# Optimization experiments

Measured on AMD Instinct MI355X. Metric: run time of the kernel, lower is better.

## Reference

```python
import math
import jax, jax.numpy as jnp
import numpy as np

jax.config.update("jax_enable_x64", True)

# ---- module hyperparameters (init_kwargs) ----
BS, NDIM, NSTEP, ORDER = 16, 16, 128, 2
NIV, NIVSTEPS = 2, 1
P = ORDER + 1                 # number of derivative channels u^(0)..u^(order)
N = NSTEP * P                 # unknowns per system
FACT = np.array([math.factorial(k) for k in range(P)], dtype=np.float64)

# Hard initial-value constraint matrix C (same sparsity for every system)
_C = np.zeros((NIVSTEPS * NIV, N), dtype=np.float64)
for _t in range(NIVSTEPS):
    for _i in range(NIV):
        _C[_t * NIV + _i, _t * P + _i] = 1.0
C = jnp.asarray(_C)
NC = C.shape[0]


def setup_inputs() -> dict:
    key = jax.random.key(0)
    k1, k2, k3, k4 = jax.random.split(key, 4)
    coeffs = jax.random.normal(k1, (BS, NDIM, NSTEP, P), dtype=jnp.float32)
    rhs = jax.random.normal(k2, (BS, NDIM, NSTEP), dtype=jnp.float32)
    iv_rhs = jax.random.normal(k3, (BS, NDIM, NIVSTEPS, NIV), dtype=jnp.float32)
    # step sizes must be positive; keep them in [0.1, 0.2] for good conditioning
    steps = 0.1 + 0.1 * jax.random.uniform(k4, (BS, NDIM, NSTEP - 1), dtype=jnp.float32)
    return {"coeffs": coeffs, "rhs": rhs, "iv_rhs": iv_rhs, "steps": steps}


def _build_A(coeffs, h):
    """Soft-constraint matrix for one scalar ODE system.
    coeffs: (NSTEP, P) f64   ODE coefficients per step
    h:      (NSTEP-1,) f64   step sizes
    Rows: [equation | fwd/bwd Taylor smoothness per order | top-order diff].
    Smoothness rows are normalized by the local truncation error h^(order+1-i).
    """
    n = NSTEP
    t = jnp.arange(n - 1)
    # equation constraints: sum_i c[t,i] u[t,i] = rhs[t]
    A_eq = jnp.zeros((n, N)).at[jnp.repeat(jnp.arange(n), P), jnp.arange(N)].set(coeffs.ravel())
    blocks = [A_eq]
    for i in range(ORDER):
        scale = h ** (-(ORDER + 1 - i))          # (n-1,)
        Af = jnp.zeros((n - 1, N))
        Ab = jnp.zeros((n - 1, N))
        for j in range(i, P):
            cf = (h ** (j - i)) / FACT[j - i]
            cb = ((-h) ** (j - i)) / FACT[j - i]
            Af = Af.at[t, t * P + j].set(scale * cf)        # forward Taylor from step t
            Ab = Ab.at[t, (t + 1) * P + j].set(scale * cb)  # backward Taylor from step t+1
        Af = Af.at[t, (t + 1) * P + i].set(-scale)
        Ab = Ab.at[t, t * P + i].set(-scale)
        blocks += [Af, Ab]
    # highest derivative varies slowly: (u[t+1,K] - u[t,K]) / h ~ 0
    Atop = (jnp.zeros((n - 1, N))
            .at[t, (t + 1) * P + ORDER].set(1.0 / h)
            .at[t, t * P + ORDER].set(-1.0 / h))
    blocks.append(Atop)
    return jnp.concatenate(blocks, axis=0)   # (m, N), m = n + 2(n-1)K + (n-1)


def _solve_one(coeffs, rhs, iv, h):
    """min ||A u - b||^2  s.t.  C u = iv  (KKT solve), one system."""
    A = _build_A(coeffs, h)
    m = A.shape[0]
    b = jnp.concatenate([rhs, jnp.zeros(m - NSTEP)])
    G = A.T @ A                                  # (N, N) banded normal matrix
    Atb = A.T @ b
    M = jnp.block([[G, C.T], [C, jnp.zeros((NC, NC))]])
    v = jnp.concatenate([Atb, iv.ravel()])
    x = jnp.linalg.solve(M, v)
    return x[:N].reshape(NSTEP, P)


def reference(coeffs, rhs, iv_rhs, steps):
    coeffs64 = coeffs.reshape(BS, NDIM, NSTEP, P).astype(jnp.float64)
    rhs64 = rhs.reshape(BS, NDIM, NSTEP).astype(jnp.float64)
    iv64 = iv_rhs.reshape(BS, NDIM, NIVSTEPS, NIV).astype(jnp.float64)
    h64 = steps.reshape(BS, NDIM, NSTEP - 1).astype(jnp.float64)
    solve = jax.vmap(jax.vmap(_solve_one))
    u = solve(coeffs64, rhs64, iv64, h64)        # (BS, NDIM, NSTEP, P)
    u0, u1, u2 = u[..., 0], u[..., 1], u[..., 2]
    return (u0, u1, u2, jnp.zeros(()), h64.reshape(BS * NDIM, NSTEP - 1, 1))
```

## Files before the change

### kernel.cpp

```cpp
#include <hip/hip_runtime.h>

#define NSYS_ 256

__device__ __forceinline__ void sym_inv3(const double D[9], double Dinv[9]) {
    const double a = D[0], b = D[3], c = D[4], d = D[6], e = D[7], f = D[8];
    const double A00 = c*f - e*e;
    const double A01 = d*e - b*f;
    const double A02 = b*e - c*d;
    const double A11 = a*f - d*d;
    const double A12 = b*d - a*e;
    const double A22 = a*c - b*b;
    const double det  = a*A00 + b*A01 + d*A02;
    const double idet = 1.0 / det;
    Dinv[0] = A00*idet; Dinv[1] = A01*idet; Dinv[2] = A02*idet;
    Dinv[3] = A01*idet; Dinv[4] = A11*idet; Dinv[5] = A12*idet;
    Dinv[6] = A02*idet; Dinv[7] = A12*idet; Dinv[8] = A22*idet;
}

__device__ __forceinline__ void iface_rows(double h, double wL[5][3], double wR[5][3]) {
    const double ih = 1.0 / h;
    const double s1 = ih * ih;
    const double s0 = s1 * ih;
    const double hh = 0.5 * ih;
    wL[0][0]= s0; wL[0][1]= s1; wL[0][2]= hh;  wR[0][0]=-s0; wR[0][1]=0.0; wR[0][2]=0.0;
    wL[1][0]=-s0; wL[1][1]=0.0; wL[1][2]=0.0;  wR[1][0]= s0; wR[1][1]=-s1; wR[1][2]= hh;
    wL[2][0]=0.0; wL[2][1]= s1; wL[2][2]= ih;  wR[2][0]=0.0; wR[2][1]=-s1; wR[2][2]=0.0;
    wL[3][0]=0.0; wL[3][1]=-s1; wL[3][2]=0.0;  wR[3][0]=0.0; wR[3][1]= s1; wR[3][2]=-ih;
    wL[4][0]=0.0; wL[4][1]=0.0; wL[4][2]=-ih;  wR[4][0]=0.0; wR[4][1]=0.0; wR[4][2]= ih;
}

__global__ __launch_bounds__(64)
void ode_pcr_1wave(const float* __restrict__ coeffs,
                   const float* __restrict__ rhs,
                   const float* __restrict__ ivr,
                   const float* __restrict__ steps,
                   float* __restrict__ out)
{
    const int sys = blockIdx.x;
    const int l   = threadIdx.x;
    const int m0  = 2*l, m1 = 2*l+1;

    const float* cP  = coeffs + (size_t)sys * 384;
    const float* rP  = rhs    + (size_t)sys * 128;
    const float* ivP = ivr    + (size_t)sys * 2;
    const float* hP  = steps  + (size_t)sys * 127;

    __shared__ double ex[2][18][64];

    const float hf0 = hP[m0];
    const float hf1 = (l < 63) ? hP[m1] : 0.0f;

    double D0[9], U0[9], r0[3], D1[9], U1[9], r1[3];
    {
        const double c0[3] = {(double)cP[m0*3+0], (double)cP[m0*3+1], (double)cP[m0*3+2]};
        const double c1[3] = {(double)cP[m1*3+0], (double)cP[m1*3+1], (double)cP[m1*3+2]};
        const double rv0 = (double)rP[m0], rv1 = (double)rP[m1];
        #pragma unroll
        for (int a=0;a<3;++a){
          #pragma unroll
          for (int b=0;b<3;++b){ D0[a*3+b]=c0[a]*c0[b]; D1[a*3+b]=c1[a]*c1[b];
                                 U0[a*3+b]=0.0;        U1[a*3+b]=0.0; }
          r0[a]=c0[a]*rv0; r1[a]=c1[a]*rv1;
        }
    }
    {
        double wL[5][3], wR[5][3];
        iface_rows((double)hf0, wL, wR);
        #pragma unroll
        for (int k=0;k<5;++k)
          #pragma unroll
          for (int a=0;a<3;++a)
            #pragma unroll
            for (int b=0;b<3;++b){
              D0[a*3+b] += wL[k][a]*wL[k][b];
              U0[a*3+b] += wL[k][a]*wR[k][b];
              D1[a*3+b] += wR[k][a]*wR[k][b];
            }
    }
    if (l >= 1) {
        double wL[5][3], wR[5][3];
        iface_rows((double)hP[m0-1], wL, wR);
        #pragma unroll
        for (int k=0;k<5;++k)
          #pragma unroll
          for (int a=0;a<3;++a)
            #pragma unroll
            for (int b=0;b<3;++b)
              D0[a*3+b] += wR[k][a]*wR[k][b];
    }
    if (l < 63) {
        double wL[5][3], wR[5][3];
        iface_rows((double)hf1, wL, wR);
        #pragma unroll
        for (int k=0;k<5;++k)
          #pragma unroll
          for (int a=0;a<3;++a)
            #pragma unroll
            for (int b=0;b<3;++b){
              D1[a*3+b] += wL[k][a]*wL[k][b];
              U1[a*3+b] += wL[k][a]*wR[k][b];
            }
    }
    if (l == 0) {
        const double iv0 = (double)ivP[0], iv1 = (double)ivP[1];
        #pragma unroll
        for (int b=0;b<3;++b) r1[b] -= U0[0*3+b]*iv0 + U0[1*3+b]*iv1;
        #pragma unroll
        for (int b=0;b<3;++b){ U0[0*3+b]=0.0; U0[1*3+b]=0.0; }
        r0[2] -= D0[6]*iv0 + D0[7]*iv1;
        r0[0] = iv0; r0[1] = iv1;
        D0[1]=D0[2]=D0[3]=D0[5]=D0[6]=D0[7]=0.0;
        D0[0]=1.0; D0[4]=1.0;
    }

    double TA[9], TB[9], z1[3];
    {
        double Dinv1[9]; sym_inv3(D1, Dinv1);
        #pragma unroll
        for (int a=0;a<3;++a)
          #pragma unroll
          for (int k=0;k<3;++k){
            double s=0.0, s2=0.0;
            #pragma unroll
            for (int j=0;j<3;++j){ s  += U0[a*3+j]*Dinv1[j*3+k];
                                   s2 += Dinv1[a*3+j]*U1[j*3+k]; }
            TA[a*3+k]=s; TB[a*3+k]=s2;
          }
        #pragma unroll
        for (int j=0;j<3;++j)
          z1[j] = Dinv1[j*3+0]*r1[0] + Dinv1[j*3+1]*r1[1] + Dinv1[j*3+2]*r1[2];
    }
    double D[9], U[9], r[3];
    #pragma unroll
    for (int a=0;a<3;++a){
      #pragma unroll
      for (int b=0;b<3;++b){
        double sd=0.0, su=0.0;
        #pragma unroll
        for (int j=0;j<3;++j){ sd += TA[a*3+j]*U0[b*3+j];
                               su += TA[a*3+j]*U1[j*3+b]; }
        D[a*3+b] = D0[a*3+b] - sd;
        U[a*3+b] = -su;
      }
      r[a] = r0[a] - (TA[a*3+0]*r1[0] + TA[a*3+1]*r1[1] + TA[a*3+2]*r1[2]);
    }
    {
        double Cn[9], cn[3];
        #pragma unroll
        for (int a=0;a<3;++a){
          #pragma unroll
          for (int b=0;b<3;++b){
            double s=0.0;
            #pragma unroll
            for (int j=0;j<3;++j) s += U1[j*3+a]*TB[j*3+b];
            Cn[a*3+b]=s;
          }
          cn[a] = U1[0*3+a]*z1[0] + U1[1*3+a]*z1[1] + U1[2*3+a]*z1[2];
        }
        ex[0][0][l]=Cn[0]; ex[0][1][l]=Cn[1]; ex[0][2][l]=Cn[2];
        ex[0][3][l]=Cn[4]; ex[0][4][l]=Cn[5]; ex[0][5][l]=Cn[8];
        ex[0][6][l]=cn[0]; ex[0][7][l]=cn[1]; ex[0][8][l]=cn[2];
    }
    __syncthreads();
    if (l >= 1) {
        const int p = l-1;
        const double C0=ex[0][0][p], C1=ex[0][1][p], C2=ex[0][2][p],
                     C3=ex[0][3][p], C4=ex[0][4][p], C5=ex[0][5][p];
        D[0]-=C0; D[1]-=C1; D[2]-=C2;
        D[3]-=C1; D[4]-=C3; D[5]-=C4;
        D[6]-=C2; D[7]-=C4; D[8]-=C5;
        r[0]-=ex[0][6][p]; r[1]-=ex[0][7][p]; r[2]-=ex[0][8][p];
    }
    __syncthreads();

    int s = 0;
    for (int d = 1; d < 64; d <<= 1, ++s) {
        double Dinv[9]; sym_inv3(D, Dinv);
        double (*buf)[64] = ex[s & 1];
        buf[0][l]=Dinv[0]; buf[1][l]=Dinv[1]; buf[2][l]=Dinv[2];
        buf[3][l]=Dinv[4]; buf[4][l]=Dinv[5]; buf[5][l]=Dinv[8];
        #pragma unroll
        for (int i=0;i<9;++i) buf[6+i][l]=U[i];
        buf[15][l]=r[0]; buf[16][l]=r[1]; buf[17][l]=r[2];
        __syncthreads();

        double nD[9], nU[9], nr[3];
        #pragma unroll
        for (int i=0;i<9;++i){ nD[i]=D[i]; nU[i]=0.0; }
        nr[0]=r[0]; nr[1]=r[1]; nr[2]=r[2];

        if (l + d < 64) {
            const int p = l + d;
            double Dp[9], Up[9], rp[3];
            Dp[0]=buf[0][p]; Dp[1]=buf[1][p]; Dp[2]=buf[2][p];
            Dp[3]=Dp[1];     Dp[4]=buf[3][p]; Dp[5]=buf[4][p];
            Dp[6]=Dp[2];     Dp[7]=Dp[5];     Dp[8]=buf[5][p];
            #pragma unroll
            for (int i=0;i<9;++i) Up[i]=buf[6+i][p];
            rp[0]=buf[15][p]; rp[1]=buf[16][p]; rp[2]=buf[17][p];
            double Tp[9];
            #pragma unroll
            for (int a=0;a<3;++a)
              #pragma unroll
              for (int k=0;k<3;++k)
                Tp[a*3+k] = U[a*3+0]*Dp[0*3+k] + U[a*3+1]*Dp[1*3+k] + U[a*3+2]*Dp[2*3+k];
            #pragma unroll
            for (int a=0;a<3;++a){
              #pragma unroll
              for (int b=0;b<3;++b){
                double su=0.0, sd=0.0;
                #pragma unroll
                for (int j=0;j<3;++j){ su += Tp[a*3+j]*Up[j*3+b]; sd += Tp[a*3+j]*U[b*3+j]; }
                nU[a*3+b] = -su;
                nD[a*3+b] -= sd;
              }
              nr[a] -= Tp[a*3+0]*rp[0] + Tp[a*3+1]*rp[1] + Tp[a*3+2]*rp[2];
            }
        }
        if (l - d >= 0) {
            const int p = l - d;
            double Dm[9], Um[9], rm[3];
            Dm[0]=buf[0][p]; Dm[1]=buf[1][p]; Dm[2]=buf[2][p];
            Dm[3]=Dm[1];     Dm[4]=buf[3][p]; Dm[5]=buf[4][p];
            Dm[6]=Dm[2];     Dm[7]=Dm[5];     Dm[8]=buf[5][p];
            #pragma unroll
            for (int i=0;i<9;++i) Um[i]=buf[6+i][p];
            rm[0]=buf[15][p]; rm[1]=buf[16][p]; rm[2]=buf[17][p];
            double Tm[9];
            #pragma unroll
            for (int a=0;a<3;++a)
              #pragma unroll
              for (int k=0;k<3;++k)
                Tm[a*3+k] = Um[0*3+a]*Dm[0*3+k] + Um[1*3+a]*Dm[1*3+k] + Um[2*3+a]*Dm[2*3+k];
            #pragma unroll
            for (int a=0;a<3;++a){
              #pragma unroll
              for (int b=0;b<3;++b){
                double sd=0.0;
                #pragma unroll
                for (int j=0;j<3;++j) sd += Tm[a*3+j]*Um[j*3+b];
                nD[a*3+b] -= sd;
              }
              nr[a] -= Tm[a*3+0]*rm[0] + Tm[a*3+1]*rm[1] + Tm[a*3+2]*rm[2];
            }
        }
        #pragma unroll
        for (int i=0;i<9;++i){ D[i]=nD[i]; U[i]=nU[i]; }
        r[0]=nr[0]; r[1]=nr[1]; r[2]=nr[2];
    }

    double Dinv[9]; sym_inv3(D, Dinv);
    const double xe0 = Dinv[0]*r[0] + Dinv[1]*r[1] + Dinv[2]*r[2];
    const double xe1 = Dinv[3]*r[0] + Dinv[4]*r[1] + Dinv[5]*r[2];
    const double xe2 = Dinv[6]*r[0] + Dinv[7]*r[1] + Dinv[8]*r[2];
    ex[0][0][l]=xe0; ex[0][1][l]=xe1; ex[0][2][l]=xe2;
    __syncthreads();
    double xN[3] = {0.0, 0.0, 0.0};
    if (l < 63) { xN[0]=ex[0][0][l+1]; xN[1]=ex[0][1][l+1]; xN[2]=ex[0][2][l+1]; }
    double xo[3];
    #pragma unroll
    for (int j=0;j<3;++j)
        xo[j] = z1[j] - (TA[0*3+j]*xe0 + TA[1*3+j]*xe1 + TA[2*3+j]*xe2)
                      - (TB[j*3+0]*xN[0] + TB[j*3+1]*xN[1] + TB[j*3+2]*xN[2]);

    float2* o0 = (float2*)(out)         + (size_t)sys*64;
    float2* o1 = (float2*)(out + 32768) + (size_t)sys*64;
    float2* o2 = (float2*)(out + 65536) + (size_t)sys*64;
    o0[l] = make_float2((float)xe0, (float)xo[0]);
    o1[l] = make_float2((float)xe1, (float)xo[1]);
    o2[l] = make_float2((float)xe2, (float)xo[2]);
    float* outH = out + 98305 + (size_t)sys*127;
    outH[m0] = hf0;
    if (l < 63) outH[m1] = hf1;
    if (sys == 0 && l == 0) out[98304] = 0.0f;
}

extern "C" void kernel_launch(void* const* d_in, const int* in_sizes, int n_in,
                              void* d_out, int out_size, void* d_ws, size_t ws_size,
                              hipStream_t stream) {
    const float* coeffs = (const float*)d_in[0];
    const float* rhs    = (const float*)d_in[1];
    const float* ivr    = (const float*)d_in[2];
    const float* steps  = (const float*)d_in[3];
    float* out = (float*)d_out;
    (void)in_sizes; (void)n_in; (void)out_size; (void)d_ws; (void)ws_size;
    hipLaunchKernelGGL(ode_pcr_1wave, dim3(NSYS_), dim3(64), 0, stream,
                       coeffs, rhs, ivr, steps, out);
}
```

Before: 12.05 us.

## Exploit symmetry, fast reciprocal, wave shuffles, and skip last-step U update in PCR

Replaces the double-precision divisions with a hardware reciprocal refined by two Newton steps, and computes only the lower triangle of the symmetric diagonal blocks. The initial interface reduction and the final back-substitution now exchange values with wave shuffles instead of shared memory and barriers. The last PCR level skips the off-diagonal update it does not need, and the step-size output is written early. These cut FP64 arithmetic and synchronisation cost; the risks are slightly different rounding and reliance on a 64-lane wave.

After: 12.12 us. About the same (+0.6%).

```diff
diff --git a/kernel.cpp b/kernel.cpp
--- a/kernel.cpp
+++ b/kernel.cpp
@@ -1,6 +1,16 @@
 #include <hip/hip_runtime.h>
+#include <math.h>
 
 #define NSYS_ 256
+
+__device__ __forceinline__ double frcp(double x) {
+    double r = __builtin_amdgcn_rcp(x);
+    double e = fma(-x, r, 1.0);
+    r = fma(r, e, r);
+    e = fma(-x, r, 1.0);
+    r = fma(r, e, r);
+    return r;
+}
 
 __device__ __forceinline__ void sym_inv3(const double D[9], double Dinv[9]) {
     const double a = D[0], b = D[3], c = D[4], d = D[6], e = D[7], f = D[8];
@@ -11,14 +21,14 @@
     const double A12 = b*d - a*e;
     const double A22 = a*c - b*b;
     const double det  = a*A00 + b*A01 + d*A02;
-    const double idet = 1.0 / det;
+    const double idet = frcp(det);
     Dinv[0] = A00*idet; Dinv[1] = A01*idet; Dinv[2] = A02*idet;
-    Dinv[3] = A01*idet; Dinv[4] = A11*idet; Dinv[5] = A12*idet;
-    Dinv[6] = A02*idet; Dinv[7] = A12*idet; Dinv[8] = A22*idet;
+    Dinv[3] = Dinv[1];  Dinv[4] = A11*idet; Dinv[5] = A12*idet;
+    Dinv[6] = Dinv[2];  Dinv[7] = Dinv[5];  Dinv[8] = A22*idet;
 }
 
 __device__ __forceinline__ void iface_rows(double h, double wL[5][3], double wR[5][3]) {
-    const double ih = 1.0 / h;
+    const double ih = frcp(h);
     const double s1 = ih * ih;
     const double s0 = s1 * ih;
     const double hh = 0.5 * ih;
@@ -50,6 +60,13 @@
     const float hf0 = hP[m0];
     const float hf1 = (l < 63) ? hP[m1] : 0.0f;
 
+    {
+        float* outH = out + 98305 + (size_t)sys*127;
+        outH[m0] = hf0;
+        if (l < 63) outH[m1] = hf1;
+        if (sys == 0 && l == 0) out[98304] = 0.0f;
+    }
+
     double D0[9], U0[9], r0[3], D1[9], U1[9], r1[3];
     {
         const double c0[3] = {(double)cP[m0*3+0], (double)cP[m0*3+1], (double)cP[m0*3+2]};
@@ -58,8 +75,9 @@
         #pragma unroll
         for (int a=0;a<3;++a){
           #pragma unroll
-          for (int b=0;b<3;++b){ D0[a*3+b]=c0[a]*c0[b]; D1[a*3+b]=c1[a]*c1[b];
-                                 U0[a*3+b]=0.0;        U1[a*3+b]=0.0; }
+          for (int b=0;b<=a;++b){ D0[a*3+b]=c0[a]*c0[b]; D1[a*3+b]=c1[a]*c1[b]; }
+          #pragma unroll
+          for (int b=0;b<3;++b){ U0[a*3+b]=0.0; U1[a*3+b]=0.0; }
           r0[a]=c0[a]*rv0; r1[a]=c1[a]*rv1;
         }
     }
@@ -69,13 +87,16 @@
         #pragma unroll
         for (int k=0;k<5;++k)
           #pragma unroll
-          for (int a=0;a<3;++a)
-            #pragma unroll
-            for (int b=0;b<3;++b){
+          for (int a=0;a<3;++a){
+            #pragma unroll
+            for (int b=0;b<=a;++b){
               D0[a*3+b] += wL[k][a]*wL[k][b];
-              U0[a*3+b] += wL[k][a]*wR[k][b];
               D1[a*3+b] += wR[k][a]*wR[k][b];
             }
+            #pragma unroll
+            for (int b=0;b<3;++b)
+              U0[a*3+b] += wL[k][a]*wR[k][b];
+          }
     }
     if (l >= 1) {
         double wL[5][3], wR[5][3];
@@ -85,7 +106,7 @@
           #pragma unroll
           for (int a=0;a<3;++a)
             #pragma unroll
-            for (int b=0;b<3;++b)
+            for (int b=0;b<=a;++b)
               D0[a*3+b] += wR[k][a]*wR[k][b];
     }
     if (l < 63) {
@@ -94,12 +115,14 @@
         #pragma unroll
         for (int k=0;k<5;++k)
           #pragma unroll
-          for (int a=0;a<3;++a)
-            #pragma unroll
-            for (int b=0;b<3;++b){
+          for (int a=0;a<3;++a){
+            #pragma unroll
+            for (int b=0;b<=a;++b)
               D1[a*3+b] += wL[k][a]*wL[k][b];
+            #pragma unroll
+            for (int b=0;b<3;++b)
               U1[a*3+b] += wL[k][a]*wR[k][b];
-            }
+          }
     }
     if (l == 0) {
         const double iv0 = (double)ivP[0], iv1 = (double)ivP[1];
@@ -109,7 +132,7 @@
         for (int b=0;b<3;++b){ U0[0*3+b]=0.0; U0[1*3+b]=0.0; }
         r0[2] -= D0[6]*iv0 + D0[7]*iv1;
         r0[0] = iv0; r0[1] = iv1;
-        D0[1]=D0[2]=D0[3]=D0[5]=D0[6]=D0[7]=0.0;
+        D0[3]=0.0; D0[6]=0.0; D0[7]=0.0;
         D0[0]=1.0; D0[4]=1.0;
     }
 
@@ -120,11 +143,8 @@
         for (int a=0;a<3;++a)
           #pragma unroll
           for (int k=0;k<3;++k){
-            double s=0.0, s2=0.0;
-            #pragma unroll
-            for (int j=0;j<3;++j){ s  += U0[a*3+j]*Dinv1[j*3+k];
-                                   s2 += Dinv1[a*3+j]*U1[j*3+k]; }
-            TA[a*3+k]=s; TB[a*3+k]=s2;
+            TA[a*3+k] = U0[a*3+0]*Dinv1[0*3+k] + U0[a*3+1]*Dinv1[1*3+k] + U0[a*3+2]*Dinv1[2*3+k];
+            TB[a*3+k] = Dinv1[a*3+0]*U1[0*3+k] + Dinv1[a*3+1]*U1[1*3+k] + Dinv1[a*3+2]*U1[2*3+k];
           }
         #pragma unroll
         for (int j=0;j<3;++j)
@@ -134,47 +154,36 @@
     #pragma unroll
     for (int a=0;a<3;++a){
       #pragma unroll
-      for (int b=0;b<3;++b){
-        double sd=0.0, su=0.0;
-        #pragma unroll
-        for (int j=0;j<3;++j){ sd += TA[a*3+j]*U0[b*3+j];
-                               su += TA[a*3+j]*U1[j*3+b]; }
-        D[a*3+b] = D0[a*3+b] - sd;
-        U[a*3+b] = -su;
-      }
+      for (int b=0;b<=a;++b)
+        D[a*3+b] = D0[a*3+b] - (TA[a*3+0]*U0[b*3+0] + TA[a*3+1]*U0[b*3+1] + TA[a*3+2]*U0[b*3+2]);
+      #pragma unroll
+      for (int b=0;b<3;++b)
+        U[a*3+b] = -(TA[a*3+0]*U1[0*3+b] + TA[a*3+1]*U1[1*3+b] + TA[a*3+2]*U1[2*3+b]);
       r[a] = r0[a] - (TA[a*3+0]*r1[0] + TA[a*3+1]*r1[1] + TA[a*3+2]*r1[2]);
     }
     {
-        double Cn[9], cn[3];
-        #pragma unroll
-        for (int a=0;a<3;++a){
-          #pragma unroll
-          for (int b=0;b<3;++b){
-            double s=0.0;
-            #pragma unroll
-            for (int j=0;j<3;++j) s += U1[j*3+a]*TB[j*3+b];
-            Cn[a*3+b]=s;
-          }
-          cn[a] = U1[0*3+a]*z1[0] + U1[1*3+a]*z1[1] + U1[2*3+a]*z1[2];
-        }
-        ex[0][0][l]=Cn[0]; ex[0][1][l]=Cn[1]; ex[0][2][l]=Cn[2];
-        ex[0][3][l]=Cn[4]; ex[0][4][l]=Cn[5]; ex[0][5][l]=Cn[8];
-        ex[0][6][l]=cn[0]; ex[0][7][l]=cn[1]; ex[0][8][l]=cn[2];
-    }
-    __syncthreads();
-    if (l >= 1) {
-        const int p = l-1;
-        const double C0=ex[0][0][p], C1=ex[0][1][p], C2=ex[0][2][p],
-                     C3=ex[0][3][p], C4=ex[0][4][p], C5=ex[0][5][p];
-        D[0]-=C0; D[1]-=C1; D[2]-=C2;
-        D[3]-=C1; D[4]-=C3; D[5]-=C4;
-        D[6]-=C2; D[7]-=C4; D[8]-=C5;
-        r[0]-=ex[0][6][p]; r[1]-=ex[0][7][p]; r[2]-=ex[0][8][p];
-    }
-    __syncthreads();
-
-    int s = 0;
-    for (int d = 1; d < 64; d <<= 1, ++s) {
+        double q[9];
+        q[0] = U1[0]*TB[0] + U1[3]*TB[3] + U1[6]*TB[6];
+        q[1] = U1[1]*TB[0] + U1[4]*TB[3] + U1[7]*TB[6];
+        q[2] = U1[2]*TB[0] + U1[5]*TB[3] + U1[8]*TB[6];
+        q[3] = U1[1]*TB[1] + U1[4]*TB[4] + U1[7]*TB[7];
+        q[4] = U1[2]*TB[1] + U1[5]*TB[4] + U1[8]*TB[7];
+        q[5] = U1[2]*TB[2] + U1[5]*TB[5] + U1[8]*TB[8];
+        q[6] = U1[0]*z1[0] + U1[3]*z1[1] + U1[6]*z1[2];
+        q[7] = U1[1]*z1[0] + U1[4]*z1[1] + U1[7]*z1[2];
+        q[8] = U1[2]*z1[0] + U1[5]*z1[1] + U1[8]*z1[2];
+        double qi[9];
+        #pragma unroll
+        for (int i=0;i<9;++i) qi[i] = __shfl_up(q[i], 1);
+        if (l >= 1) {
+            D[0]-=qi[0]; D[3]-=qi[1]; D[6]-=qi[2]; D[4]-=qi[3]; D[7]-=qi[4]; D[8]-=qi[5];
+            r[0]-=qi[6]; r[1]-=qi[7]; r[2]-=qi[8];
+        }
+    }
+
+    #pragma unroll 1
+    for (int s = 0; s < 6; ++s) {
+        const int d = 1 << s;
         double Dinv[9]; sym_inv3(D, Dinv);
         double (*buf)[64] = ex[s & 1];
         buf[0][l]=Dinv[0]; buf[1][l]=Dinv[1]; buf[2][l]=Dinv[2];
@@ -184,68 +193,76 @@
         buf[15][l]=r[0]; buf[16][l]=r[1]; buf[17][l]=r[2];
         __syncthreads();
 
-        double nD[9], nU[9], nr[3];
-        #pragma unroll
-        for (int i=0;i<9;++i){ nD[i]=D[i]; nU[i]=0.0; }
-        nr[0]=r[0]; nr[1]=r[1]; nr[2]=r[2];
+        double nD[6] = { D[0], D[3], D[6], D[4], D[7], D[8] };
+        double nU[9];
+        #pragma unroll
+        for (int i=0;i<9;++i) nU[i]=0.0;
+        double nr[3] = { r[0], r[1], r[2] };
 
         if (l + d < 64) {
             const int p = l + d;
-            double Dp[9], Up[9], rp[3];
+            double Dp[9];
             Dp[0]=buf[0][p]; Dp[1]=buf[1][p]; Dp[2]=buf[2][p];
             Dp[3]=Dp[1];     Dp[4]=buf[3][p]; Dp[5]=buf[4][p];
             Dp[6]=Dp[2];     Dp[7]=Dp[5];     Dp[8]=buf[5][p];
-            #pragma unroll
-            for (int i=0;i<9;++i) Up[i]=buf[6+i][p];
-            rp[0]=buf[15][p]; rp[1]=buf[16][p]; rp[2]=buf[17][p];
-            double Tp[9];
+            const double rp0=buf[15][p], rp1=buf[16][p], rp2=buf[17][p];
+            double T[9];
             #pragma unroll
             for (int a=0;a<3;++a)
               #pragma unroll
               for (int k=0;k<3;++k)
-                Tp[a*3+k] = U[a*3+0]*Dp[0*3+k] + U[a*3+1]*Dp[1*3+k] + U[a*3+2]*Dp[2*3+k];
-            #pragma unroll
-            for (int a=0;a<3;++a){
-              #pragma unroll
-              for (int b=0;b<3;++b){
-                double su=0.0, sd=0.0;
+                T[a*3+k] = U[a*3+0]*Dp[0*3+k] + U[a*3+1]*Dp[1*3+k] + U[a*3+2]*Dp[2*3+k];
+            nD[0] -= T[0]*U[0] + T[1]*U[1] + T[2]*U[2];
+            nD[1] -= T[3]*U[0] + T[4]*U[1] + T[5]*U[2];
+            nD[2] -= T[6]*U[0] + T[7]*U[1] + T[8]*U[2];
+            nD[3] -= T[3]*U[3] + T[4]*U[4] + T[5]*U[5];
+            nD[4] -= T[6]*U[3] + T[7]*U[4] + T[8]*U[5];
+            nD[5] -= T[6]*U[6] + T[7]*U[7] + T[8]*U[8];
+            nr[0] -= T[0]*rp0 + T[1]*rp1 + T[2]*rp2;
+            nr[1] -= T[3]*rp0 + T[4]*rp1 + T[5]*rp2;
+            nr[2] -= T[6]*rp0 + T[7]*rp1 + T[8]*rp2;
+            if (s < 5) {
+                double Up[9];
                 #pragma unroll
-                for (int j=0;j<3;++j){ su += Tp[a*3+j]*Up[j*3+b]; sd += Tp[a*3+j]*U[b*3+j]; }
-                nU[a*3+b] = -su;
-                nD[a*3+b] -= sd;
-              }
-              nr[a] -= Tp[a*3+0]*rp[0] + Tp[a*3+1]*rp[1] + Tp[a*3+2]*rp[2];
+                for (int i=0;i<9;++i) Up[i]=buf[6+i][p];
+                #pragma unroll
+                for (int a=0;a<3;++a)
+                  #pragma unroll
+                  for (int b=0;b<3;++b)
+                    nU[a*3+b] = -(T[a*3+0]*Up[0*3+b] + T[a*3+1]*Up[1*3+b] + T[a*3+2]*Up[2*3+b]);
             }
         }
-        if (l - d >= 0) {
+        if (l >= d) {
             const int p = l - d;
-            double Dm[9], Um[9], rm[3];
+            double Dm[9];
             Dm[0]=buf[0][p]; Dm[1]=buf[1][p]; Dm[2]=buf[2][p];
             Dm[3]=Dm[1];     Dm[4]=buf[3][p]; Dm[5]=buf[4][p];
             Dm[6]=Dm[2];     Dm[7]=Dm[5];     Dm[8]=buf[5][p];
+            double Um[9];
             #pragma unroll
             for (int i=0;i<9;++i) Um[i]=buf[6+i][p];
-            rm[0]=buf[15][p]; rm[1]=buf[16][p]; rm[2]=buf[17][p];
+            const double rm0=buf[15][p], rm1=buf[16][p], rm2=buf[17][p];
             double Tm[9];
             #pragma unroll
             for (int a=0;a<3;++a)
               #pragma unroll
               for (int k=0;k<3;++k)
                 Tm[a*3+k] = Um[0*3+a]*Dm[0*3+k] + Um[1*3+a]*Dm[1*3+k] + Um[2*3+a]*Dm[2*3+k];
-            #pragma unroll
-            for (int a=0;a<3;++a){
-              #pragma unroll
-              for (int b=0;b<3;++b){
-                double sd=0.0;
-                #pragma unroll
-                for (int j=0;j<3;++j) sd += Tm[a*3+j]*Um[j*3+b];
-                nD[a*3+b] -= sd;
-              }
-              nr[a] -= Tm[a*3+0]*rm[0] + Tm[a*3+1]*rm[1] + Tm[a*3+2]*rm[2];
-            }
-        }
-        #pragma unroll
-        for (int i=0;i<9;++i){ D[i]=nD[i]; U[i]=nU[i]; }
+            nD[0] -= Tm[0]*Um[0] + Tm[1]*Um[3] + Tm[2]*Um[6];
+            nD[1] -= Tm[3]*Um[0] + Tm[4]*Um[3] + Tm[5]*Um[6];
+            nD[2] -= Tm[6]*Um[0] + Tm[7]*Um[3] + Tm[8]*Um[6];
+            nD[3] -= Tm[3]*Um[1] + Tm[4]*Um[4] + Tm[5]*Um[7];
+            nD[4] -= Tm[6]*Um[1] + Tm[7]*Um[4] + Tm[8]*Um[7];
+            nD[5] -= Tm[6]*Um[2] + Tm[7]*Um[5] + Tm[8]*Um[8];
+            nr[0] -= Tm[0]*rm0 + Tm[1]*rm1 + Tm[2]*rm2;
+            nr[1] -= Tm[3]*rm0 + Tm[4]*rm1 + Tm[5]*rm2;
+            nr[2] -= Tm[6]*rm0 + Tm[7]*rm1 + Tm[8]*rm2;
+        }
+        D[0]=nD[0]; D[3]=nD[1]; D[6]=nD[2]; D[4]=nD[3]; D[7]=nD[4]; D[8]=nD[5];
+        if (s < 5) {
+            #pragma unroll
+            for (int i=0;i<9;++i) U[i]=nU[i];
+        }
         r[0]=nr[0]; r[1]=nr[1]; r[2]=nr[2];
     }
 
@@ -253,15 +270,15 @@
     const double xe0 = Dinv[0]*r[0] + Dinv[1]*r[1] + Dinv[2]*r[2];
     const double xe1 = Dinv[3]*r[0] + Dinv[4]*r[1] + Dinv[5]*r[2];
     const double xe2 = Dinv[6]*r[0] + Dinv[7]*r[1] + Dinv[8]*r[2];
-    ex[0][0][l]=xe0; ex[0][1][l]=xe1; ex[0][2][l]=xe2;
-    __syncthreads();
-    double xN[3] = {0.0, 0.0, 0.0};
-    if (l < 63) { xN[0]=ex[0][0][l+1]; xN[1]=ex[0][1][l+1]; xN[2]=ex[0][2][l+1]; }
+    double xN0 = __shfl_down(xe0, 1);
+    double xN1 = __shfl_down(xe1, 1);
+    double xN2 = __shfl_down(xe2, 1);
+    if (l == 63) { xN0 = 0.0; xN1 = 0.0; xN2 = 0.0; }
     double xo[3];
     #pragma unroll
     for (int j=0;j<3;++j)
         xo[j] = z1[j] - (TA[0*3+j]*xe0 + TA[1*3+j]*xe1 + TA[2*3+j]*xe2)
-                      - (TB[j*3+0]*xN[0] + TB[j*3+1]*xN[1] + TB[j*3+2]*xN[2]);
+                      - (TB[j*3+0]*xN0 + TB[j*3+1]*xN1 + TB[j*3+2]*xN2);
 
     float2* o0 = (float2*)(out)         + (size_t)sys*64;
     float2* o1 = (float2*)(out + 32768) + (size_t)sys*64;
@@ -269,10 +286,6 @@
     o0[l] = make_float2((float)xe0, (float)xo[0]);
     o1[l] = make_float2((float)xe1, (float)xo[1]);
     o2[l] = make_float2((float)xe2, (float)xo[2]);
-    float* outH = out + 98305 + (size_t)sys*127;
-    outH[m0] = hf0;
-    if (l < 63) outH[m1] = hf1;
-    if (sys == 0 && l == 0) out[98304] = 0.0f;
 }
 
 extern "C" void kernel_launch(void* const* d_in, const int* in_sizes, int n_in,
```
